# Kernel tuning notes

Measured on AMD Instinct MI355X. Metric: run time of the kernel, lower is better.

## Reference

```python
import jax, jax.numpy as jnp
import numpy as np

OUT_FEATURES = 4096
IN_FEATURES = 4096
R = 16
DIST = 4
N_FREQ = 10000
SCALING = 150.0


def setup_inputs() -> dict:
    key = jax.random.key(0)
    k_x, k_w, k_b, k_s, k_a, k_i = jax.random.split(key, 6)
    x = jax.random.normal(k_x, (4, 2048, IN_FEATURES), dtype=jnp.float32)
    base_w = jax.random.normal(k_w, (OUT_FEATURES, IN_FEATURES), dtype=jnp.float32) * 0.02
    base_b = jax.random.normal(k_b, (OUT_FEATURES,), dtype=jnp.float32) * 0.02
    spectrum = jax.random.normal(k_s, (N_FREQ,), dtype=jnp.float32)
    hora_A = jax.random.normal(k_a, (R, IN_FEATURES), dtype=jnp.float32)
    # torch uses randperm(r*out_features)[:n_frequency] -> unique flat indices
    idx = jax.random.permutation(k_i, R * OUT_FEATURES)[:N_FREQ].astype(jnp.int32)
    return {"x": x, "base_w": base_w, "base_b": base_b,
            "spectrum": spectrum, "hora_A": hora_A, "idx": idx}


def reference(x, base_w, base_b, spectrum, hora_A, idx):
    # --- get_delta_weight ---
    rows = idx // R            # index into out_features
    cols = idx % R             # index into r
    dense_spectrum = jnp.zeros((OUT_FEATURES, R), dtype=spectrum.dtype)
    dense_spectrum = dense_spectrum.at[rows, cols].set(spectrum)
    # chunk_size = ceil(out/dist) = 1024; out divisible by dist -> pure reshape
    chunks = dense_spectrum.reshape(DIST, OUT_FEATURES // DIST, R)
    B = jnp.fft.ifft2(chunks, axes=(-2, -1)).real.astype(spectrum.dtype)
    B = B.reshape(OUT_FEATURES, R)
    delta_w = (B * SCALING) @ hora_A          # [out_features, in_features]
    # --- forward: base linear + adapter linear ---
    base_out = jnp.einsum('bsi,oi->bso', x, base_w) + base_b
    result = base_out + jnp.einsum('bsi,oi->bso', x, delta_w)
    return result
```

## Files before the change

### kernel.cpp

```cpp
#include <hip/hip_runtime.h>
#include <hip/hip_bf16.h>


#define OUTF 4096
#define INF  4096
#define NFREQ 10000
#define MDIM 8192
#define KT   (INF / 64)

typedef __attribute__((ext_vector_type(8))) short bf16x8;
typedef __attribute__((ext_vector_type(4))) float f32x4;

__device__ __forceinline__ unsigned int bf16pack2(float a, float b) {
    unsigned int ua = __builtin_bit_cast(unsigned int, a);
    unsigned int ub = __builtin_bit_cast(unsigned int, b);
    ua = (ua + 0x7fffu + ((ua >> 16) & 1u)) >> 16;
    ub = (ub + 0x7fffu + ((ub >> 16) & 1u)) & 0xffff0000u;
    return ua | ub;
}

__device__ __forceinline__ void async_copy16(const void* g, void* l) {
    __builtin_amdgcn_global_load_lds(
        (__attribute__((address_space(1))) void*)(g),
        (__attribute__((address_space(3))) void*)(l),
        16, 0, 0);
}

__global__ __launch_bounds__(256) void compact_sort_kernel(
        const float* __restrict__ spectrum, const int* __restrict__ idx,
        int2* __restrict__ cjk2, int* __restrict__ boff) {
    const int p   = blockIdx.x;
    const int tid = threadIdx.x;
    const int wv  = tid >> 6, ln = tid & 63;
    __shared__ int2 s_list[4096];
    __shared__ int  wcnt[4];
    __shared__ int  s_cnt;
    __shared__ int  kcnt[16];
    __shared__ int  kbase[17];
    int cnt = 0;
    for (int i0 = wv * 64; i0 < NFREQ; i0 += 256) {
        const int i = i0 + ln;
        bool m = (i < NFREQ) && ((idx[i] >> 14) == p);
        cnt += __popcll(__ballot(m));
    }
    if (ln == 0) wcnt[wv] = cnt;
    __syncthreads();
    int base = 0;
    for (int w = 0; w < wv; ++w) base += wcnt[w];
    for (int i0 = wv * 64; i0 < NFREQ; i0 += 256) {
        const int i = i0 + ln;
        bool m = false; int id = 0;
        if (i < NFREQ) { id = idx[i]; m = ((id >> 14) == p); }
        unsigned long long bal = __ballot(m);
        if (m) {
            int pos = base + __popcll(bal & ((1ull << ln) - 1ull));
            if (pos < 4096)
                s_list[pos] = make_int2(id & 16383,
                                        __builtin_bit_cast(int, spectrum[i]));
        }
        base += __popcll(bal);
    }
    if (tid == 0) {
        int t = wcnt[0] + wcnt[1] + wcnt[2] + wcnt[3];
        s_cnt = (t < 4096) ? t : 4096;
    }
    __syncthreads();
    const int n = s_cnt;
    for (int q = 0; q < 4; ++q) {
        const int k = wv * 4 + q;
        int c = 0;
        for (int t0 = 0; t0 < n; t0 += 64) {
            const int t = t0 + ln;
            bool m = (t < n) && ((s_list[t].x & 15) == k);
            c += __popcll(__ballot(m));
        }
        if (ln == 0) kcnt[k] = c;
    }
    __syncthreads();
    if (tid == 0) {
        int a = 0;
        for (int k = 0; k < 16; ++k) { kbase[k] = a; a += kcnt[k]; }
        kbase[16] = a;
    }
    __syncthreads();
    for (int q = 0; q < 4; ++q) {
        const int k = wv * 4 + q;
        int b2 = kbase[k];
        for (int t0 = 0; t0 < n; t0 += 64) {
            const int t = t0 + ln;
            bool m = (t < n) && ((s_list[t].x & 15) == k);
            unsigned long long bal = __ballot(m);
            if (m) {
                int pos = b2 + __popcll(bal & ((1ull << ln) - 1ull));
                cjk2[p * 4096 + pos] = make_int2(s_list[t].x >> 4, s_list[t].y);
            }
            b2 += __popcll(bal);
        }
    }
    if (tid < 17) boff[p * 17 + tid] = kbase[tid];
}

__global__ __launch_bounds__(256) void buildB_cvt_kernel(
        const int2* __restrict__ cjk2, const int* __restrict__ boff,
        float* __restrict__ Bout,
        const float4* __restrict__ x4, uint2* __restrict__ xb) {
    __shared__ int2  s_jv[4096];
    __shared__ float s1re[16][16];
    __shared__ float s1im[16][17];
    if (blockIdx.x < 256) {
        const int tid  = threadIdx.x;
        const int p    = blockIdx.x >> 6;
        const int mblk = blockIdx.x & 63;
        const int cnt  = boff[p * 17 + 16];
        for (int t = tid; t < cnt; t += 256) s_jv[t] = cjk2[p * 4096 + t];
        __syncthreads();
        const int m_loc = tid >> 4;
        const int k     = tid & 15;
        const int m     = mblk * 16 + m_loc;
        const int kb0   = boff[p * 17 + k];
        const int kb1   = boff[p * 17 + k + 1];
        const float c1  = 6.283185307179586f / 1024.f;
        float re = 0.f, im = 0.f;
        for (int t = kb0; t < kb1; ++t) {
            const int2 jv = s_jv[t];
            const float v = __builtin_bit_cast(float, jv.y);
            const float ang = (float)((jv.x * m) & 1023) * c1;
            re += v * __cosf(ang);
            im += v * __sinf(ang);
        }
        s1re[m_loc][k] = re;
        s1im[m_loc][k] = im;
        __syncthreads();
        const int r = k;
        const float c2 = 6.283185307179586f / 16.f;
        float b = 0.f;
#pragma unroll
        for (int k2 = 0; k2 < 16; ++k2) {
            const float ang = (float)((k2 * r) & 15) * c2;
            b += s1re[m_loc][k2] * __cosf(ang) - s1im[m_loc][k2] * __sinf(ang);
        }
        const int o = p * 1024 + m;
        Bout[o * 16 + r] = b * (150.f / 16384.f);
    }
    const int n4 = (MDIM * INF) / 4;
    for (int i = blockIdx.x * 256 + threadIdx.x; i < n4; i += 2048 * 256) {
        float4 v = x4[i];
        xb[i] = make_uint2(bf16pack2(v.x, v.y), bf16pack2(v.z, v.w));
    }
}

__global__ __launch_bounds__(256) void build_w_kernel(
        const float* __restrict__ bw, const float* __restrict__ A,
        const float* __restrict__ Bs, unsigned short* __restrict__ W) {
    const int n0 = blockIdx.x * 8;
    __shared__ float sB[8][16];
    if (threadIdx.x < 128)
        ((float*)sB)[threadIdx.x] = Bs[n0 * 16 + threadIdx.x];
    __syncthreads();
    const float4* A4 = (const float4*)A;
    const float4* bw4 = (const float4*)bw;
    uint2* W2 = (uint2*)W;
#pragma unroll 1
    for (int q = 0; q < 4; ++q) {
        const int c4 = threadIdx.x + q * 256;
        float4 a[16];
#pragma unroll
        for (int r = 0; r < 16; ++r) a[r] = A4[r * 1024 + c4];
#pragma unroll 1
        for (int nn = 0; nn < 8; ++nn) {
            const int n = n0 + nn;
            float4 wv = bw4[n * 1024 + c4];
#pragma unroll
            for (int r = 0; r < 16; ++r) {
                float s = sB[nn][r];
                wv.x += s * a[r].x; wv.y += s * a[r].y;
                wv.z += s * a[r].z; wv.w += s * a[r].w;
            }
            W2[n * 1024 + c4] = make_uint2(bf16pack2(wv.x, wv.y),
                                           bf16pack2(wv.z, wv.w));
        }
    }
}

__global__ __launch_bounds__(512, 2) void gemm256_kernel(
        const unsigned short* __restrict__ Xb,
        const unsigned short* __restrict__ Wb,
        const float* __restrict__ bias, float* __restrict__ C) {
    __shared__ __align__(1024) char lds[131072];

    const int tid  = threadIdx.x;
    const int lane = tid & 63;
    const int wid  = tid >> 6;
    const int wm   = wid >> 2;
    const int wn   = wid & 3;

    int bid = blockIdx.x;
    bid = (bid & 7) * 64 + (bid >> 3);
    const int tm = bid >> 4;
    const int tn = bid & 15;
    const int arow0 = tm * 256;
    const int brow0 = tn * 256;

    const int srow  = tid >> 3;
    const int scole = (((tid & 7) * 16) ^ ((srow & 7) << 4)) >> 1;
    const int sldsb = tid * 16;

    const int l15 = lane & 15;
    const int kx0 = ((lane >> 4) * 16) ^ ((lane & 7) << 4);
    const int kx1 = kx0 ^ 64;
    const int abase0 = (wm * 128 + l15) * 128;
    const int bbase0 = 32768 + (wn * 64 + l15) * 128;

    f32x4 acc[8][4] = {};
    bf16x8 af[4][2], bfa[2][2], bfb[2][2];

#define STAGE_HALF(mat, grow0, t, ldsbase) do {                               \
        const unsigned short* _s =                                            \
            (mat) + ((grow0) + srow) * INF + (t) * 64 + scole;                \
        async_copy16(_s, lds + (ldsbase) + sldsb);                            \
        async_copy16(_s + 64 * INF, lds + (ldsbase) + 8192 + sldsb);          \
    } while (0)

#define LDA(DB, m, kh) (*(const bf16x8*)(lds + (DB) + abase0 + (m) * 2048 + ((kh) ? kx1 : kx0)))
#define LDB(DB, n, kh) (*(const bf16x8*)(lds + (DB) + bbase0 + (n) * 2048 + ((kh) ? kx1 : kx0)))
#define MFMA(a, b, c) __builtin_amdgcn_mfma_f32_16x16x32_bf16((a), (b), (c), 0, 0, 0)
#define BARRIER() do { asm volatile("" ::: "memory");                         \
                       __builtin_amdgcn_s_barrier();                          \
                       asm volatile("" ::: "memory"); } while (0)
#define LGKM0()  asm volatile("s_waitcnt lgkmcnt(0)" ::: "memory")

#define QMFMA(mh, BF)                                                         \
    __builtin_amdgcn_s_setprio(1);                                            \
    _Pragma("unroll") for (int ks = 0; ks < 2; ++ks)                          \
        _Pragma("unroll") for (int m = 0; m < 4; ++m)                         \
            _Pragma("unroll") for (int n = 0; n < 2; ++n)                     \
                acc[(mh) * 4 + m][(BF) * 2 + n] =                             \
                    MFMA(af[m][ks], ((BF) ? bfb : bfa)[n][ks],                \
                         acc[(mh) * 4 + m][(BF) * 2 + n]);                    \
    __builtin_amdgcn_s_setprio(0)

#define RD_AF(DB, mh)                                                         \
    _Pragma("unroll") for (int m = 0; m < 4; ++m) {                           \
        af[m][0] = LDA(DB, (mh) * 4 + m, 0);                                  \
        af[m][1] = LDA(DB, (mh) * 4 + m, 1); }
#define RD_BFA(DB)                                                            \
    _Pragma("unroll") for (int n = 0; n < 2; ++n) {                           \
        bfa[n][0] = LDB(DB, n, 0); bfa[n][1] = LDB(DB, n, 1); }
#define RD_BFB(DB)                                                            \
    _Pragma("unroll") for (int n = 0; n < 2; ++n) {                           \
        bfb[n][0] = LDB(DB, n + 2, 0); bfb[n][1] = LDB(DB, n + 2, 1); }

#define PAIR(CUR, OTH, s) do {                                                \
                         \
    RD_AF(CUR, 0);                                                            \
    STAGE_HALF(Xb, arow0 + 128, (s) + 1, (OTH) + 16384);                      \
    BARRIER(); LGKM0(); QMFMA(0, 0); BARRIER();                               \
                        \
    RD_BFB(CUR);                                                              \
    STAGE_HALF(Wb, brow0 + 128, (s) + 1, (OTH) + 49152);                      \
    BARRIER(); LGKM0(); QMFMA(0, 1); BARRIER();                               \
                        \
    RD_AF(CUR, 1);                                                            \
    if ((s) + 2 < KT) STAGE_HALF(Wb, brow0, (s) + 2, (CUR) + 32768);          \
    BARRIER(); LGKM0(); QMFMA(1, 0); BARRIER();                               \
                \
    if ((s) + 2 < KT) {                                                       \
        STAGE_HALF(Xb, arow0, (s) + 2, (CUR) + 0);                            \
        asm volatile("s_waitcnt vmcnt(4)" ::: "memory");                      \
    } else { asm volatile("s_waitcnt vmcnt(0)" ::: "memory"); }               \
    BARRIER();                                                                \
    RD_BFA(OTH);                                                              \
    QMFMA(1, 1); BARRIER();                                                   \
                        \
    RD_AF(OTH, 0);                                                            \
    if ((s) + 2 < KT) STAGE_HALF(Xb, arow0 + 128, (s) + 2, (CUR) + 16384);    \
    BARRIER(); LGKM0(); QMFMA(0, 0); BARRIER();                               \
                       \
    RD_BFB(OTH);                                                              \
    if ((s) + 2 < KT) STAGE_HALF(Wb, brow0 + 128, (s) + 2, (CUR) + 49152);    \
    BARRIER(); LGKM0(); QMFMA(0, 1); BARRIER();                               \
                       \
    RD_AF(OTH, 1);                                                            \
    if ((s) + 3 < KT) STAGE_HALF(Wb, brow0, (s) + 3, (OTH) + 32768);          \
    BARRIER(); LGKM0(); QMFMA(1, 0); BARRIER();                               \
    \
    if ((s) + 3 < KT) {                                                       \
        STAGE_HALF(Xb, arow0, (s) + 3, (OTH) + 0);                            \
        asm volatile("s_waitcnt vmcnt(4)" ::: "memory");                      \
    } else { asm volatile("s_waitcnt vmcnt(0)" ::: "memory"); }               \
    BARRIER();                                                                \
    if ((s) + 2 < KT) { RD_BFA(CUR); }                                        \
    QMFMA(1, 1); BARRIER();                                                   \
} while (0)

    STAGE_HALF(Wb, brow0,       0, 32768);
    STAGE_HALF(Xb, arow0,       0, 0);
    STAGE_HALF(Xb, arow0 + 128, 0, 16384);
    STAGE_HALF(Wb, brow0 + 128, 0, 49152);
    STAGE_HALF(Wb, brow0,       1, 65536 + 32768);
    STAGE_HALF(Xb, arow0,       1, 65536 + 0);
    asm volatile("s_waitcnt vmcnt(4)" ::: "memory");
    BARRIER();
    RD_BFA(0);

    for (int s = 0; s < KT; s += 2)
        PAIR(0, 65536, s);

#pragma unroll
    for (int n = 0; n < 4; ++n) {
        const int gcol = brow0 + wn * 64 + n * 16 + l15;
        const float bv = bias[gcol];
#pragma unroll
        for (int m = 0; m < 8; ++m) {
            const int grow = arow0 + wm * 128 + m * 16 + (lane >> 4) * 4;
#pragma unroll
            for (int rg = 0; rg < 4; ++rg)
                C[(grow + rg) * OUTF + gcol] = acc[m][n][rg] + bv;
        }
    }
#undef STAGE_HALF
#undef LDA
#undef LDB
#undef MFMA
#undef BARRIER
#undef LGKM0
#undef QMFMA
#undef RD_AF
#undef RD_BFA
#undef RD_BFB
#undef PAIR
}

extern "C" void kernel_launch(void* const* d_in, const int* in_sizes, int n_in,
                              void* d_out, int out_size, void* d_ws, size_t ws_size,
                              hipStream_t stream) {
    const float* x    = (const float*)d_in[0];
    const float* bw   = (const float*)d_in[1];
    const float* bb   = (const float*)d_in[2];
    const float* spec = (const float*)d_in[3];
    const float* ha   = (const float*)d_in[4];
    const int*   idx  = (const int*)d_in[5];
    float* out = (float*)d_out;

    char* ws = (char*)d_ws;
    float*          Bbuf = (float*)ws;
    unsigned short* Wb   = (unsigned short*)(ws + 262144);
    unsigned short* Xb   = (unsigned short*)(ws + 262144 + 33554432);
    int2*           cjk2 = (int2*)(ws + 262144 + 33554432 + 67108864);
    int*            boff = (int*)(ws + 262144 + 33554432 + 67108864 + 131072);

    compact_sort_kernel<<<4, 256, 0, stream>>>(spec, idx, cjk2, boff);
    buildB_cvt_kernel<<<2048, 256, 0, stream>>>(cjk2, boff, Bbuf,
                                                (const float4*)x, (uint2*)Xb);
    build_w_kernel<<<512, 256, 0, stream>>>(bw, ha, Bbuf, Wb);
    gemm256_kernel<<<512, 512, 0, stream>>>(Xb, Wb, bb, out);
}
```

Measured before the change: 388.1 us.

## Apply low-rank adapter as xA·Bᵀ epilogue instead of materializing delta weight

Drops the kernel that built W = base_w + B·A in fp32 before bf16 conversion. base_w and hora_A are now converted to bf16 in one streaming kernel, and a small MFMA kernel computes xA = X·Aᵀ (8192x16). The main GEMM's epilogue adds one rank-16 MFMA step (zero-padded to K=32) using xA and B before the bias store. This removes the dense rank-16 update over the full weight, but it adds a pass that rereads bf16 X and rounds xA and B to bf16, which changes numerics.

```diff
diff --git a/kernel.cpp b/kernel.cpp
--- a/kernel.cpp
+++ b/kernel.cpp
@@ -7,6 +7,9 @@
 #define NFREQ 10000
 #define MDIM 8192
 #define KT   (INF / 64)
+#define NX4  ((MDIM * INF) / 4)
+#define NW4  ((OUTF * INF) / 4)
+#define NA4  ((16 * INF) / 4)
 
 typedef __attribute__((ext_vector_type(8))) short bf16x8;
 typedef __attribute__((ext_vector_type(4))) float f32x4;
@@ -19,11 +22,27 @@
     return ua | ub;
 }
 
+__device__ __forceinline__ short bf16of(float f) {
+    unsigned int u = __builtin_bit_cast(unsigned int, f);
+    u = (u + 0x7fffu + ((u >> 16) & 1u)) >> 16;
+    return (short)u;
+}
+
 __device__ __forceinline__ void async_copy16(const void* g, void* l) {
     __builtin_amdgcn_global_load_lds(
         (__attribute__((address_space(1))) void*)(g),
         (__attribute__((address_space(3))) void*)(l),
         16, 0, 0);
+}
+
+__device__ __forceinline__ bf16x8 pad_frag16(const float* rowp, int kg) {
+    bf16x8 v = (bf16x8){0, 0, 0, 0, 0, 0, 0, 0};
+    if (kg < 2) {
+        const float* q = rowp + kg * 8;
+#pragma unroll
+        for (int j = 0; j < 8; ++j) v[j] = bf16of(q[j]);
+    }
+    return v;
 }
 
 __global__ __launch_bounds__(256) void compact_sort_kernel(
@@ -100,84 +119,89 @@
     if (tid < 17) boff[p * 17 + tid] = kbase[tid];
 }
 
-__global__ __launch_bounds__(256) void buildB_cvt_kernel(
+__global__ __launch_bounds__(256) void buildB_kernel(
         const int2* __restrict__ cjk2, const int* __restrict__ boff,
-        float* __restrict__ Bout,
-        const float4* __restrict__ x4, uint2* __restrict__ xb) {
+        float* __restrict__ Bout) {
     __shared__ int2  s_jv[4096];
     __shared__ float s1re[16][16];
     __shared__ float s1im[16][17];
-    if (blockIdx.x < 256) {
-        const int tid  = threadIdx.x;
-        const int p    = blockIdx.x >> 6;
-        const int mblk = blockIdx.x & 63;
-        const int cnt  = boff[p * 17 + 16];
-        for (int t = tid; t < cnt; t += 256) s_jv[t] = cjk2[p * 4096 + t];
-        __syncthreads();
-        const int m_loc = tid >> 4;
-        const int k     = tid & 15;
-        const int m     = mblk * 16 + m_loc;
-        const int kb0   = boff[p * 17 + k];
-        const int kb1   = boff[p * 17 + k + 1];
-        const float c1  = 6.283185307179586f / 1024.f;
-        float re = 0.f, im = 0.f;
-        for (int t = kb0; t < kb1; ++t) {
-            const int2 jv = s_jv[t];
-            const float v = __builtin_bit_cast(float, jv.y);
-            const float ang = (float)((jv.x * m) & 1023) * c1;
-            re += v * __cosf(ang);
-            im += v * __sinf(ang);
-        }
-        s1re[m_loc][k] = re;
-        s1im[m_loc][k] = im;
-        __syncthreads();
-        const int r = k;
-        const float c2 = 6.283185307179586f / 16.f;
-        float b = 0.f;
-#pragma unroll
-        for (int k2 = 0; k2 < 16; ++k2) {
-            const float ang = (float)((k2 * r) & 15) * c2;
-            b += s1re[m_loc][k2] * __cosf(ang) - s1im[m_loc][k2] * __sinf(ang);
-        }
-        const int o = p * 1024 + m;
-        Bout[o * 16 + r] = b * (150.f / 16384.f);
-    }
-    const int n4 = (MDIM * INF) / 4;
-    for (int i = blockIdx.x * 256 + threadIdx.x; i < n4; i += 2048 * 256) {
-        float4 v = x4[i];
-        xb[i] = make_uint2(bf16pack2(v.x, v.y), bf16pack2(v.z, v.w));
-    }
-}
-
-__global__ __launch_bounds__(256) void build_w_kernel(
-        const float* __restrict__ bw, const float* __restrict__ A,
-        const float* __restrict__ Bs, unsigned short* __restrict__ W) {
-    const int n0 = blockIdx.x * 8;
-    __shared__ float sB[8][16];
-    if (threadIdx.x < 128)
-        ((float*)sB)[threadIdx.x] = Bs[n0 * 16 + threadIdx.x];
-    __syncthreads();
-    const float4* A4 = (const float4*)A;
-    const float4* bw4 = (const float4*)bw;
-    uint2* W2 = (uint2*)W;
-#pragma unroll 1
-    for (int q = 0; q < 4; ++q) {
-        const int c4 = threadIdx.x + q * 256;
-        float4 a[16];
-#pragma unroll
-        for (int r = 0; r < 16; ++r) a[r] = A4[r * 1024 + c4];
-#pragma unroll 1
-        for (int nn = 0; nn < 8; ++nn) {
-            const int n = n0 + nn;
-            float4 wv = bw4[n * 1024 + c4];
-#pragma unroll
-            for (int r = 0; r < 16; ++r) {
-                float s = sB[nn][r];
-                wv.x += s * a[r].x; wv.y += s * a[r].y;
-                wv.z += s * a[r].z; wv.w += s * a[r].w;
-            }
-            W2[n * 1024 + c4] = make_uint2(bf16pack2(wv.x, wv.y),
-                                           bf16pack2(wv.z, wv.w));
+    const int tid  = threadIdx.x;
+    const int p    = blockIdx.x >> 6;
+    const int mblk = blockIdx.x & 63;
+    const int cnt  = boff[p * 17 + 16];
+    for (int t = tid; t < cnt; t += 256) s_jv[t] = cjk2[p * 4096 + t];
+    __syncthreads();
+    const int m_loc = tid >> 4;
+    const int k     = tid & 15;
+    const int m     = mblk * 16 + m_loc;
+    const int kb0   = boff[p * 17 + k];
+    const int kb1   = boff[p * 17 + k + 1];
+    const float c1  = 6.283185307179586f / 1024.f;
+    float re = 0.f, im = 0.f;
+    for (int t = kb0; t < kb1; ++t) {
+        const int2 jv = s_jv[t];
+        const float v = __builtin_bit_cast(float, jv.y);
+        const float ang = (float)((jv.x * m) & 1023) * c1;
+        re += v * __cosf(ang);
+        im += v * __sinf(ang);
+    }
+    s1re[m_loc][k] = re;
+    s1im[m_loc][k] = im;
+    __syncthreads();
+    const int r = k;
+    const float c2 = 6.283185307179586f / 16.f;
+    float b = 0.f;
+#pragma unroll
+    for (int k2 = 0; k2 < 16; ++k2) {
+        const float ang = (float)((k2 * r) & 15) * c2;
+        b += s1re[m_loc][k2] * __cosf(ang) - s1im[m_loc][k2] * __sinf(ang);
+    }
+    Bout[(p * 1024 + m) * 16 + r] = b * (150.f / 16384.f);
+}
+
+__global__ __launch_bounds__(256) void cvt_stream_kernel(
+        const float4* __restrict__ x4,  uint2* __restrict__ xb,
+        const float4* __restrict__ bw4, uint2* __restrict__ wbb,
+        const float4* __restrict__ a4,  uint2* __restrict__ ab) {
+    const int stride = 2048 * 256;
+    for (int i = blockIdx.x * 256 + threadIdx.x; i < NX4 + NW4 + NA4;
+         i += stride) {
+        float4 v; uint2* d;
+        if (i < NX4)            { v = x4[i];              d = xb + i; }
+        else if (i < NX4 + NW4) { v = bw4[i - NX4];       d = wbb + (i - NX4); }
+        else                    { v = a4[i - NX4 - NW4];  d = ab + (i - NX4 - NW4); }
+        *d = make_uint2(bf16pack2(v.x, v.y), bf16pack2(v.z, v.w));
+    }
+}
+
+__global__ __launch_bounds__(256) void xa_kernel(
+        const unsigned short* __restrict__ Xb,
+        const unsigned short* __restrict__ Ab,
+        float* __restrict__ xA) {
+    __shared__ float s_acc[4][64][4];
+    const int tid  = threadIdx.x;
+    const int lane = tid & 63;
+    const int wv   = tid >> 6;
+    const int l15  = lane & 15;
+    const int kg   = lane >> 4;
+    const int row0 = blockIdx.x * 16;
+    const int k0   = wv * 1024;
+    f32x4 acc = {};
+#pragma unroll 8
+    for (int kk = 0; kk < 1024; kk += 32) {
+        bf16x8 af = *(const bf16x8*)&Xb[(row0 + l15) * INF + k0 + kk + kg * 8];
+        bf16x8 bf = *(const bf16x8*)&Ab[l15 * INF + k0 + kk + kg * 8];
+        acc = __builtin_amdgcn_mfma_f32_16x16x32_bf16(af, bf, acc, 0, 0, 0);
+    }
+#pragma unroll
+    for (int r = 0; r < 4; ++r) s_acc[wv][lane][r] = acc[r];
+    __syncthreads();
+    if (tid < 64) {
+#pragma unroll
+        for (int r = 0; r < 4; ++r) {
+            float s = s_acc[0][tid][r] + s_acc[1][tid][r] +
+                      s_acc[2][tid][r] + s_acc[3][tid][r];
+            xA[(row0 + (tid >> 4) * 4 + r) * 16 + (tid & 15)] = s;
         }
     }
 }
@@ -185,7 +209,10 @@
 __global__ __launch_bounds__(512, 2) void gemm256_kernel(
         const unsigned short* __restrict__ Xb,
         const unsigned short* __restrict__ Wb,
-        const float* __restrict__ bias, float* __restrict__ C) {
+        const float* __restrict__ bias,
+        const float* __restrict__ xA,
+        const float* __restrict__ Bsp,
+        float* __restrict__ C) {
     __shared__ __align__(1024) char lds[131072];
 
     const int tid  = threadIdx.x;
@@ -251,19 +278,15 @@
         bfb[n][0] = LDB(DB, n + 2, 0); bfb[n][1] = LDB(DB, n + 2, 1); }
 
 #define PAIR(CUR, OTH, s) do {                                                \
-                         \
     RD_AF(CUR, 0);                                                            \
     STAGE_HALF(Xb, arow0 + 128, (s) + 1, (OTH) + 16384);                      \
     BARRIER(); LGKM0(); QMFMA(0, 0); BARRIER();                               \
-                        \
     RD_BFB(CUR);                                                              \
     STAGE_HALF(Wb, brow0 + 128, (s) + 1, (OTH) + 49152);                      \
     BARRIER(); LGKM0(); QMFMA(0, 1); BARRIER();                               \
-                        \
     RD_AF(CUR, 1);                                                            \
     if ((s) + 2 < KT) STAGE_HALF(Wb, brow0, (s) + 2, (CUR) + 32768);          \
     BARRIER(); LGKM0(); QMFMA(1, 0); BARRIER();                               \
-                \
     if ((s) + 2 < KT) {                                                       \
         STAGE_HALF(Xb, arow0, (s) + 2, (CUR) + 0);                            \
         asm volatile("s_waitcnt vmcnt(4)" ::: "memory");                      \
@@ -271,19 +294,15 @@
     BARRIER();                                                                \
     RD_BFA(OTH);                                                              \
     QMFMA(1, 1); BARRIER();                                                   \
-                        \
     RD_AF(OTH, 0);                                                            \
     if ((s) + 2 < KT) STAGE_HALF(Xb, arow0 + 128, (s) + 2, (CUR) + 16384);    \
     BARRIER(); LGKM0(); QMFMA(0, 0); BARRIER();                               \
-                       \
     RD_BFB(OTH);                                                              \
     if ((s) + 2 < KT) STAGE_HALF(Wb, brow0 + 128, (s) + 2, (CUR) + 49152);    \
     BARRIER(); LGKM0(); QMFMA(0, 1); BARRIER();                               \
-                       \
     RD_AF(OTH, 1);                                                            \
     if ((s) + 3 < KT) STAGE_HALF(Wb, brow0, (s) + 3, (OTH) + 32768);          \
     BARRIER(); LGKM0(); QMFMA(1, 0); BARRIER();                               \
-    \
     if ((s) + 3 < KT) {                                                       \
         STAGE_HALF(Xb, arow0, (s) + 3, (OTH) + 0);                            \
         asm volatile("s_waitcnt vmcnt(4)" ::: "memory");                      \
@@ -305,6 +324,21 @@
 
     for (int s = 0; s < KT; s += 2)
         PAIR(0, 65536, s);
+
+    {
+        const int kg = lane >> 4;
+        bf16x8 afa[8];
+#pragma unroll
+        for (int m = 0; m < 8; ++m)
+            afa[m] = pad_frag16(xA + (arow0 + wm * 128 + m * 16 + l15) * 16, kg);
+#pragma unroll
+        for (int n = 0; n < 4; ++n) {
+            bf16x8 bfr = pad_frag16(Bsp + (brow0 + wn * 64 + n * 16 + l15) * 16, kg);
+#pragma unroll
+            for (int m = 0; m < 8; ++m)
+                acc[m][n] = MFMA(afa[m], bfr, acc[m][n]);
+        }
+    }
 
 #pragma unroll
     for (int n = 0; n < 4; ++n) {
@@ -345,13 +379,18 @@
     char* ws = (char*)d_ws;
     float*          Bbuf = (float*)ws;
     unsigned short* Wb   = (unsigned short*)(ws + 262144);
-    unsigned short* Xb   = (unsigned short*)(ws + 262144 + 33554432);
-    int2*           cjk2 = (int2*)(ws + 262144 + 33554432 + 67108864);
-    int*            boff = (int*)(ws + 262144 + 33554432 + 67108864 + 131072);
+    unsigned short* Xb   = (unsigned short*)(ws + 33816576);
+    int2*           cjk2 = (int2*)(ws + 100925440);
+    int*            boff = (int*)(ws + 101056512);
+    unsigned short* Ab   = (unsigned short*)(ws + 101060608);
+    float*          xA   = (float*)(ws + 101191680);
 
     compact_sort_kernel<<<4, 256, 0, stream>>>(spec, idx, cjk2, boff);
-    buildB_cvt_kernel<<<2048, 256, 0, stream>>>(cjk2, boff, Bbuf,
-                                                (const float4*)x, (uint2*)Xb);
-    build_w_kernel<<<512, 256, 0, stream>>>(bw, ha, Bbuf, Wb);
-    gemm256_kernel<<<512, 512, 0, stream>>>(Xb, Wb, bb, out);
-}
+    buildB_kernel<<<256, 256, 0, stream>>>(cjk2, boff, Bbuf);
+    cvt_stream_kernel<<<2048, 256, 0, stream>>>(
+        (const float4*)x,  (uint2*)Xb,
+        (const float4*)bw, (uint2*)Wb,
+        (const float4*)ha, (uint2*)Ab);
+    xa_kernel<<<512, 256, 0, stream>>>(Xb, Ab, xA);
+    gemm256_kernel<<<512, 512, 0, stream>>>(Xb, Wb, bb, xA, Bbuf, out);
+}
```

Result: slower. 408.6 us (+5.3%).

## Fuse spectrum-to-B, weight build, and x bf16 conversion into one prep kernel

Applied to the files above, without the earlier changes.

Merges the B (inverse FFT) computation, the delta-weight build and the x fp32-to-bf16 conversion into a single 512-block kernel. Each block computes its 8 rows of B directly into shared memory, removing the global B buffer round trip and one kernel launch. The x conversion now runs on 512 blocks instead of 2048, which may lower memory-level parallelism for that bandwidth-bound pass. Each block also reloads the full spectrum list into shared memory.

```diff
diff --git a/kernel.cpp b/kernel.cpp
--- a/kernel.cpp
+++ b/kernel.cpp
@@ -7,6 +7,7 @@
 #define NFREQ 10000
 #define MDIM 8192
 #define KT   (INF / 64)
+#define NX4  ((MDIM * INF) / 4)
 
 typedef __attribute__((ext_vector_type(8))) short bf16x8;
 typedef __attribute__((ext_vector_type(4))) float f32x4;
@@ -100,23 +101,25 @@
     if (tid < 17) boff[p * 17 + tid] = kbase[tid];
 }
 
-__global__ __launch_bounds__(256) void buildB_cvt_kernel(
+__global__ __launch_bounds__(256) void prep_fused_kernel(
         const int2* __restrict__ cjk2, const int* __restrict__ boff,
-        float* __restrict__ Bout,
+        const float* __restrict__ bw, const float* __restrict__ A,
+        unsigned short* __restrict__ W,
         const float4* __restrict__ x4, uint2* __restrict__ xb) {
     __shared__ int2  s_jv[4096];
-    __shared__ float s1re[16][16];
-    __shared__ float s1im[16][17];
-    if (blockIdx.x < 256) {
-        const int tid  = threadIdx.x;
-        const int p    = blockIdx.x >> 6;
-        const int mblk = blockIdx.x & 63;
-        const int cnt  = boff[p * 17 + 16];
-        for (int t = tid; t < cnt; t += 256) s_jv[t] = cjk2[p * 4096 + t];
-        __syncthreads();
+    __shared__ float s1re[8][16];
+    __shared__ float s1im[8][17];
+    __shared__ float sB[8][17];
+    const int tid = threadIdx.x;
+    const int n0  = blockIdx.x * 8;
+    const int p   = n0 >> 10;
+    const int cnt = boff[p * 17 + 16];
+    for (int t = tid; t < cnt; t += 256) s_jv[t] = cjk2[p * 4096 + t];
+    __syncthreads();
+    if (tid < 128) {
         const int m_loc = tid >> 4;
         const int k     = tid & 15;
-        const int m     = mblk * 16 + m_loc;
+        const int m     = (n0 & 1023) + m_loc;
         const int kb0   = boff[p * 17 + k];
         const int kb1   = boff[p * 17 + k + 1];
         const float c1  = 6.283185307179586f / 1024.f;
@@ -130,39 +133,27 @@
         }
         s1re[m_loc][k] = re;
         s1im[m_loc][k] = im;
-        __syncthreads();
-        const int r = k;
-        const float c2 = 6.283185307179586f / 16.f;
+    }
+    __syncthreads();
+    if (tid < 128) {
+        const int m_loc = tid >> 4;
+        const int r     = tid & 15;
+        const float c2  = 6.283185307179586f / 16.f;
         float b = 0.f;
 #pragma unroll
         for (int k2 = 0; k2 < 16; ++k2) {
             const float ang = (float)((k2 * r) & 15) * c2;
             b += s1re[m_loc][k2] * __cosf(ang) - s1im[m_loc][k2] * __sinf(ang);
         }
-        const int o = p * 1024 + m;
-        Bout[o * 16 + r] = b * (150.f / 16384.f);
-    }
-    const int n4 = (MDIM * INF) / 4;
-    for (int i = blockIdx.x * 256 + threadIdx.x; i < n4; i += 2048 * 256) {
-        float4 v = x4[i];
-        xb[i] = make_uint2(bf16pack2(v.x, v.y), bf16pack2(v.z, v.w));
-    }
-}
-
-__global__ __launch_bounds__(256) void build_w_kernel(
-        const float* __restrict__ bw, const float* __restrict__ A,
-        const float* __restrict__ Bs, unsigned short* __restrict__ W) {
-    const int n0 = blockIdx.x * 8;
-    __shared__ float sB[8][16];
-    if (threadIdx.x < 128)
-        ((float*)sB)[threadIdx.x] = Bs[n0 * 16 + threadIdx.x];
-    __syncthreads();
-    const float4* A4 = (const float4*)A;
+        sB[m_loc][r] = b * (150.f / 16384.f);
+    }
+    __syncthreads();
+    const float4* A4  = (const float4*)A;
     const float4* bw4 = (const float4*)bw;
     uint2* W2 = (uint2*)W;
 #pragma unroll 1
     for (int q = 0; q < 4; ++q) {
-        const int c4 = threadIdx.x + q * 256;
+        const int c4 = tid + q * 256;
         float4 a[16];
 #pragma unroll
         for (int r = 0; r < 16; ++r) a[r] = A4[r * 1024 + c4];
@@ -179,6 +170,10 @@
             W2[n * 1024 + c4] = make_uint2(bf16pack2(wv.x, wv.y),
                                            bf16pack2(wv.z, wv.w));
         }
+    }
+    for (int i = blockIdx.x * 256 + tid; i < NX4; i += 512 * 256) {
+        float4 v = x4[i];
+        xb[i] = make_uint2(bf16pack2(v.x, v.y), bf16pack2(v.z, v.w));
     }
 }
 
@@ -251,19 +246,15 @@
         bfb[n][0] = LDB(DB, n + 2, 0); bfb[n][1] = LDB(DB, n + 2, 1); }
 
 #define PAIR(CUR, OTH, s) do {                                                \
-                         \
     RD_AF(CUR, 0);                                                            \
     STAGE_HALF(Xb, arow0 + 128, (s) + 1, (OTH) + 16384);                      \
     BARRIER(); LGKM0(); QMFMA(0, 0); BARRIER();                               \
-                        \
     RD_BFB(CUR);                                                              \
     STAGE_HALF(Wb, brow0 + 128, (s) + 1, (OTH) + 49152);                      \
     BARRIER(); LGKM0(); QMFMA(0, 1); BARRIER();                               \
-                        \
     RD_AF(CUR, 1);                                                            \
     if ((s) + 2 < KT) STAGE_HALF(Wb, brow0, (s) + 2, (CUR) + 32768);          \
     BARRIER(); LGKM0(); QMFMA(1, 0); BARRIER();                               \
-                \
     if ((s) + 2 < KT) {                                                       \
         STAGE_HALF(Xb, arow0, (s) + 2, (CUR) + 0);                            \
         asm volatile("s_waitcnt vmcnt(4)" ::: "memory");                      \
@@ -271,19 +262,15 @@
     BARRIER();                                                                \
     RD_BFA(OTH);                                                              \
     QMFMA(1, 1); BARRIER();                                                   \
-                        \
     RD_AF(OTH, 0);                                                            \
     if ((s) + 2 < KT) STAGE_HALF(Xb, arow0 + 128, (s) + 2, (CUR) + 16384);    \
     BARRIER(); LGKM0(); QMFMA(0, 0); BARRIER();                               \
-                       \
     RD_BFB(OTH);                                                              \
     if ((s) + 2 < KT) STAGE_HALF(Wb, brow0 + 128, (s) + 2, (CUR) + 49152);    \
     BARRIER(); LGKM0(); QMFMA(0, 1); BARRIER();                               \
-                       \
     RD_AF(OTH, 1);                                                            \
     if ((s) + 3 < KT) STAGE_HALF(Wb, brow0, (s) + 3, (OTH) + 32768);          \
     BARRIER(); LGKM0(); QMFMA(1, 0); BARRIER();                               \
-    \
     if ((s) + 3 < KT) {                                                       \
         STAGE_HALF(Xb, arow0, (s) + 3, (OTH) + 0);                            \
         asm volatile("s_waitcnt vmcnt(4)" ::: "memory");                      \
@@ -343,15 +330,13 @@
     float* out = (float*)d_out;
 
     char* ws = (char*)d_ws;
-    float*          Bbuf = (float*)ws;
-    unsigned short* Wb   = (unsigned short*)(ws + 262144);
-    unsigned short* Xb   = (unsigned short*)(ws + 262144 + 33554432);
-    int2*           cjk2 = (int2*)(ws + 262144 + 33554432 + 67108864);
-    int*            boff = (int*)(ws + 262144 + 33554432 + 67108864 + 131072);
+    unsigned short* Wb   = (unsigned short*)ws;
+    unsigned short* Xb   = (unsigned short*)(ws + 33554432);
+    int2*           cjk2 = (int2*)(ws + 100663296);
+    int*            boff = (int*)(ws + 100794368);
 
     compact_sort_kernel<<<4, 256, 0, stream>>>(spec, idx, cjk2, boff);
-    buildB_cvt_kernel<<<2048, 256, 0, stream>>>(cjk2, boff, Bbuf,
-                                                (const float4*)x, (uint2*)Xb);
-    build_w_kernel<<<512, 256, 0, stream>>>(bw, ha, Bbuf, Wb);
+    prep_fused_kernel<<<512, 256, 0, stream>>>(
+        cjk2, boff, bw, ha, Wb, (const float4*)x, (uint2*)Xb);
     gemm256_kernel<<<512, 512, 0, stream>>>(Xb, Wb, bb, out);
 }
```

After: 393.7 us. About the same (+1.4%).
